# Optimization experiments

Measured on AMD Instinct MI355X. Metric: run time of the kernel, lower is better.

The kernel has to match this reference:

```python
import jax, jax.numpy as jnp
import numpy as np

B, T, D, H = 4, 2048, 1024, 16
E = D // H  # 64
DH = D // 4  # sensor hidden dim


def setup_inputs() -> dict:
    key = jax.random.key(0)
    ks = jax.random.split(key, 9)
    s = D ** -0.5
    return {
        "x": jax.random.normal(ks[0], (B, T, D), jnp.float32),
        "q_w": jax.random.normal(ks[1], (D, D), jnp.float32) * s,
        "k_w": jax.random.normal(ks[2], (D, D), jnp.float32) * s,
        "v_w": jax.random.normal(ks[3], (D, D), jnp.float32) * s,
        "o_w": jax.random.normal(ks[4], (D, D), jnp.float32) * s,
        "cs_w1": jax.random.normal(ks[5], (DH, D), jnp.float32) * s,
        "cs_b1": jnp.zeros((DH,), jnp.float32),
        "cs_w2": jax.random.normal(ks[6], (H, DH), jnp.float32) * (DH ** -0.5),
        "cs_b2": jnp.zeros((H,), jnp.float32),
        "decay_params": jax.random.normal(ks[7], (H, E), jnp.float32) + 3.0,
    }


def reference(x, q_w, k_w, v_w, o_w, cs_w1, cs_b1, cs_w2, cs_b2, decay_params):
    Bx, Tx, Dx = x.shape
    # projections (torch Linear: y = x @ W.T), split into heads
    q = (x @ q_w.T).reshape(Bx, Tx, H, E)
    k = (x @ k_w.T).reshape(Bx, Tx, H, E)
    v = (x @ v_w.T).reshape(Bx, Tx, H, E)
    # complexity sensor -> per-head scalar in (0,1)
    lc = jax.nn.sigmoid(jnp.tanh(x @ cs_w1.T + cs_b1) @ cs_w2.T + cs_b2)  # [B,T,H]
    base = jax.nn.sigmoid(decay_params)[None, None]                       # [1,1,H,E]
    lam = jnp.clip(base * (1.0 + 0.2 * lc[..., None]), 0.0, 0.9995)       # [B,T,H,E]

    def step(state, inp):
        qt, kt, vt, dt = inp  # each [B,H,E]
        # S(t) = diag(dt) S(t-1) + k_t v_t^T  (decay along key dim e)
        state = state * dt[..., None] + kt[..., None] * vt[:, :, None, :]
        out_t = jnp.einsum('bhe,bhef->bhf', qt, state)
        return state, out_t

    init = jnp.zeros((Bx, H, E, E), x.dtype)
    xs = (jnp.swapaxes(q, 0, 1), jnp.swapaxes(k, 0, 1),
          jnp.swapaxes(v, 0, 1), jnp.swapaxes(lam, 0, 1))  # time-major
    _, ys = jax.lax.scan(step, init, xs)  # ys: [T,B,H,E]
    y = jnp.swapaxes(ys, 0, 1).reshape(Bx, Tx, Dx)
    return y @ o_w.T
```

## Files before the change

### kernel.cpp

```cpp
#include <hip/hip_runtime.h>

#define DEV __device__ __forceinline__
#define MFMA(a, b, c) __builtin_amdgcn_mfma_f32_16x16x32_bf16(a, b, c, 0, 0, 0)

typedef __bf16 bf16x8 __attribute__((ext_vector_type(8)));
typedef float f32x4 __attribute__((ext_vector_type(4)));
typedef unsigned short u16x8 __attribute__((ext_vector_type(8)));

DEV float blo(unsigned u) { return __builtin_bit_cast(float, u << 16); }
DEV float bhi(unsigned u) { return __builtin_bit_cast(float, u & 0xFFFF0000u); }
DEV unsigned short f2b(float f) {
  unsigned u = __builtin_bit_cast(unsigned, f);
  return (unsigned short)((u + 0x7FFFu + ((u >> 16) & 1u)) >> 16);
}
DEV unsigned cvtpk(float lo, float hi) {
  unsigned r;
  asm("v_cvt_pk_bf16_f32 %0, %1, %2" : "=v"(r) : "v"(lo), "v"(hi));
  return r;
}
DEV float sigf(float x) { return 1.0f / (1.0f + expf(-x)); }

DEV void llds16(const void* g, void* l) {
  __builtin_amdgcn_global_load_lds(
      (__attribute__((address_space(1))) void*)(void*)g,
      (__attribute__((address_space(3))) void*)l, 16, 0, 0);
}

__global__ __launch_bounds__(256) void cvt_w_kernel(
    const float* __restrict__ qw, const float* __restrict__ kw,
    const float* __restrict__ vw, const float* __restrict__ cw1,
    const float* __restrict__ ow, unsigned short* __restrict__ WCAT,
    unsigned short* __restrict__ OWB) {
  const int i = blockIdx.x * 256 + threadIdx.x;
  const float* s;
  unsigned short* d;
  if (i < 262144)      { s = qw  + (size_t)i * 4;                 d = WCAT + (size_t)i * 4; }
  else if (i < 524288) { size_t j = i - 262144; s = kw  + j * 4;  d = WCAT + 1048576 + j * 4; }
  else if (i < 786432) { size_t j = i - 524288; s = vw  + j * 4;  d = WCAT + 2097152 + j * 4; }
  else if (i < 851968) { size_t j = i - 786432; s = cw1 + j * 4;  d = WCAT + 3145728 + j * 4; }
  else if (i < 1114112){ size_t j = i - 851968; s = ow  + j * 4;  d = OWB + j * 4; }
  else return;
  float4 f = *(const float4*)s;
  ushort4 o;
  o.x = f2b(f.x); o.y = f2b(f.y); o.z = f2b(f.z); o.w = f2b(f.w);
  *(ushort4*)d = o;
}

template <int OUTF, int AF32>
__global__ __launch_bounds__(256, 2) void gemm_bk64_kernel(
    const void* __restrict__ Ap, const unsigned short* __restrict__ B,
    void* __restrict__ Cout, unsigned short* __restrict__ Cout2,
    int K, int ldC, int act_col0, const float* __restrict__ bias, int nbn) {
  __shared__ char As[16384];
  __shared__ char Bs[16384];
  const int tid = threadIdx.x;
  const int lane = tid & 63;
  const int w = tid >> 6;
  const int wr = w >> 1, wc = w & 1;
  const int ln15 = lane & 15, hi = lane >> 4;

  const int nwg = gridDim.x, orig = blockIdx.x;
  const int qd = nwg >> 3, rm = nwg & 7;
  const int xcd = orig & 7, loc = orig >> 3;
  const int swz = (xcd < rm ? xcd * (qd + 1) : rm * (qd + 1) + (xcd - rm) * qd) + loc;
  const int bn = swz % nbn, bm = swz / nbn;
  const int m0 = bm * 128, n0 = bn * 128;

  auto stage = [&](const unsigned short* src, int row0, int k0, char* dst) {
#pragma unroll
    for (int j = 0; j < 4; ++j) {
      const int slot = j * 256 + tid;
      const int rr = slot >> 3;
      const int kc = (slot & 7) ^ (rr & 7);
      llds16(src + (size_t)(row0 + rr) * K + k0 + kc * 8, dst + slot * 16);
    }
  };
  auto stageA32 = [&](const float* src, int row0, int k0, char* dst) {
    float4 f[4][2];
#pragma unroll
    for (int j = 0; j < 4; ++j) {
      const int slot = j * 256 + tid;
      const int rr = slot >> 3;
      const int kc = (slot & 7) ^ (rr & 7);
      const float* g = src + (size_t)(row0 + rr) * K + k0 + kc * 8;
      f[j][0] = *(const float4*)g;
      f[j][1] = *(const float4*)(g + 4);
    }
#pragma unroll
    for (int j = 0; j < 4; ++j) {
      const int slot = j * 256 + tid;
      uint4 o = { cvtpk(f[j][0].x, f[j][0].y), cvtpk(f[j][0].z, f[j][0].w),
                  cvtpk(f[j][1].x, f[j][1].y), cvtpk(f[j][1].z, f[j][1].w) };
      *(uint4*)(dst + slot * 16) = o;
    }
  };
  auto rd = [&](const char* unit, int row, int ks) -> bf16x8 {
    const int kc = (ks * 4 + hi) ^ (row & 7);
    return *(const bf16x8*)(unit + row * 128 + kc * 16);
  };

  f32x4 acc[4][4] = {};
  const int nk = K >> 6;
  for (int kt = 0; kt < nk; ++kt) {
    if (AF32) stageA32((const float*)Ap, m0, kt * 64, As);
    else      stage((const unsigned short*)Ap, m0, kt * 64, As);
    stage(B, n0, kt * 64, Bs);
    __syncthreads();
    bf16x8 af[2][4], bf[2][4];
#pragma unroll
    for (int ks = 0; ks < 2; ++ks)
#pragma unroll
      for (int i = 0; i < 4; ++i) {
        af[ks][i] = rd(As, wr * 64 + i * 16 + ln15, ks);
        bf[ks][i] = rd(Bs, wc * 64 + i * 16 + ln15, ks);
      }
#pragma unroll
    for (int i = 0; i < 4; ++i)
#pragma unroll
      for (int j = 0; j < 4; ++j) {
        acc[i][j] = MFMA(af[0][i], bf[0][j], acc[i][j]);
        acc[i][j] = MFMA(af[1][i], bf[1][j], acc[i][j]);
      }
    __syncthreads();
  }
#pragma unroll
  for (int i = 0; i < 4; ++i) {
    const int rowb = m0 + wr * 64 + i * 16 + hi * 4;
#pragma unroll
    for (int j = 0; j < 4; ++j) {
      const int col = n0 + wc * 64 + j * 16 + ln15;
#pragma unroll
      for (int r = 0; r < 4; ++r) {
        float v = acc[i][j][r];
        if (col >= act_col0) {
          v = tanhf(v + bias[col - act_col0]);
          Cout2[(size_t)(rowb + r) * 256 + (col - act_col0)] = f2b(v);
        } else {
          const size_t off = (size_t)(rowb + r) * ldC + col;
          if (OUTF == 0) ((unsigned short*)Cout)[off] = f2b(v);
          else ((float*)Cout)[off] = v;
        }
      }
    }
  }
}

__global__ __launch_bounds__(256) void sensor2_kernel(
    const unsigned short* __restrict__ H1, const float* __restrict__ w2,
    const float* __restrict__ b2, float* __restrict__ LC) {
  const int tid = threadIdx.x;
  const int h = tid & 15, r = tid >> 4;
  const int m = blockIdx.x * 16 + r;
  const unsigned short* hrow = H1 + (size_t)m * 256;
  const float* wrow = w2 + h * 256;
  float acc = 0.0f;
  for (int d = 0; d < 256; d += 8) {
    uint4 hv = *(const uint4*)(hrow + d);
    float4 wa = *(const float4*)(wrow + d);
    float4 wb = *(const float4*)(wrow + d + 4);
    acc = fmaf(blo(hv.x), wa.x, acc); acc = fmaf(bhi(hv.x), wa.y, acc);
    acc = fmaf(blo(hv.y), wa.z, acc); acc = fmaf(bhi(hv.y), wa.w, acc);
    acc = fmaf(blo(hv.z), wb.x, acc); acc = fmaf(bhi(hv.z), wb.y, acc);
    acc = fmaf(blo(hv.w), wb.z, acc); acc = fmaf(bhi(hv.w), wb.w, acc);
  }
  LC[(size_t)m * 16 + h] = sigf(acc + b2[h]);
}

__global__ __launch_bounds__(256) void scan_passA_kernel(
    const unsigned short* __restrict__ QKV, const float* __restrict__ LC,
    const float* __restrict__ decay, unsigned short* __restrict__ MTB,
    float* __restrict__ P) {
  __shared__ char SH[34304];
  ushort* kL = (ushort*)SH;
  ushort* vL = (ushort*)(SH + 8192);
  char* khT  = SH + 16384;
  char* vT   = SH + 24576;
  float* sigL = (float*)(SH + 32768);
  float* lcL  = (float*)(SH + 33024);
  float* Lp   = (float*)(SH + 33280);

  const int tid = threadIdx.x;
  const int c = blockIdx.x, h = blockIdx.y, b = blockIdx.z;
  const int t0 = c * 64;
#pragma unroll
  for (int i = 0; i < 2; ++i) {
    int idx = i * 256 + tid;
    int row = idx >> 3, ch = idx & 7;
    size_t g = (size_t)(b * 2048 + t0 + row) * 3072 + h * 64 + ch * 8;
    int lb = (i * 256 + (tid >> 6) * 64) * 16;
    llds16(QKV + g + 1024, (char*)kL + lb);
    llds16(QKV + g + 2048, (char*)vL + lb);
  }
  if (tid < 64) sigL[tid] = sigf(decay[h * 64 + tid]);
  else if (tid < 128) lcL[tid - 64] = LC[(size_t)(b * 2048 + t0 + tid - 64) * 16 + h];
  __syncthreads();

  const int e = tid & 63, seg = tid >> 6;
  const float sig_e = sigL[e];
  float lp = 1.f;
#pragma unroll
  for (int i = 0; i < 16; ++i)
    lp *= fminf(sig_e * (1.f + 0.2f * lcL[seg * 16 + i]), 0.9995f);
  Lp[seg * 64 + e] = lp;
  __syncthreads();
  float T = 1.f;
#pragma unroll
  for (int sg = 0; sg < 4; ++sg) if (sg > seg) T *= Lp[sg * 64 + e];

  u16x8 ka = {}, kb = {};
  float r = T;
#pragma unroll
  for (int i = 15; i >= 0; --i) {
    int s = seg * 16 + i;
    float lam = fminf(sig_e * (1.f + 0.2f * lcL[s]), 0.9995f);
    float kv = blo((unsigned)kL[s * 64 + e]) * r;
    if (i >= 8) kb[i - 8] = f2b(kv); else ka[i] = f2b(kv);
    r *= lam;
  }
  *(u16x8*)(khT + e * 128 + (((2 * seg + 0) ^ (e & 7)) * 16)) = ka;
  *(u16x8*)(khT + e * 128 + (((2 * seg + 1) ^ (e & 7)) * 16)) = kb;
  if (seg == 0) P[((size_t)((b * 16 + h) * 32 + c)) * 64 + e] = r;

  u16x8 va = {}, vb = {};
#pragma unroll
  for (int i = 0; i < 16; ++i) {
    unsigned short vv = vL[(seg * 16 + i) * 64 + e];
    if (i >= 8) vb[i - 8] = vv; else va[i] = vv;
  }
  *(u16x8*)(vT + e * 128 + (((2 * seg + 0) ^ (e & 7)) * 16)) = va;
  *(u16x8*)(vT + e * 128 + (((2 * seg + 1) ^ (e & 7)) * 16)) = vb;
  __syncthreads();

  const int ln15 = tid & 15, hi = (tid & 63) >> 4, w = tid >> 6;
  auto rd = [&](const char* u, int row, int ks) -> bf16x8 {
    return *(const bf16x8*)(u + row * 128 + (((ks * 4 + hi) ^ (row & 7)) * 16));
  };
  bf16x8 av0 = rd(vT, w * 16 + ln15, 0), av1 = rd(vT, w * 16 + ln15, 1);
  unsigned short* Mp = MTB + ((size_t)((b * 16 + h) * 32 + c)) * 4096;
#pragma unroll
  for (int er = 0; er < 4; ++er) {
    f32x4 acc = {};
    acc = MFMA(av0, rd(khT, er * 16 + ln15, 0), acc);
    acc = MFMA(av1, rd(khT, er * 16 + ln15, 1), acc);
    const int e2 = er * 16 + ln15;
#pragma unroll
    for (int rr = 0; rr < 4; ++rr) {
      const int f = w * 16 + hi * 4 + rr;
      Mp[f * 64 + (((e2 >> 3) ^ (f & 7)) << 3) + (e2 & 7)] = f2b(acc[rr]);
    }
  }
}

__global__ __launch_bounds__(256) void scan_passB_kernel(
    unsigned short* __restrict__ MTB, const float* __restrict__ P) {
  const int bh = blockIdx.y;
  const int task = blockIdx.x * 256 + threadIdx.x;
  const int f = task >> 6, slot = (task >> 3) & 7, pos = task & 7;
  const int e = ((slot ^ (f & 7)) << 3) | pos;
  const size_t base = (size_t)bh * 32;
  float S = 0.0f;
  for (int c = 0; c < 32; ++c) {
    unsigned short* Mp = MTB + (base + c) * 4096 + task;
    const float p = P[(base + c) * 64 + e];
    const float m = blo((unsigned)*Mp);
    *Mp = f2b(S);
    S = fmaf(p, S, m);
  }
}

__global__ __launch_bounds__(256) void scan_passC_kernel(
    const unsigned short* __restrict__ QKV, const float* __restrict__ LC,
    const float* __restrict__ decay, const unsigned short* __restrict__ MTB,
    unsigned short* __restrict__ Y) {
  __shared__ char SH[50688];
  ushort* qL = (ushort*)SH;
  ushort* kL = (ushort*)(SH + 8192);
  ushort* vL = (ushort*)(SH + 16384);
  char* qT = SH + 24576;
  char* kT = SH + 32768;
  char* vT = SH + 40960;
  char* Ab   = SH;
  char* sinT = SH + 8192;
  float* sigL = (float*)(SH + 49152);
  float* lcL  = (float*)(SH + 49408);
  float* Lp   = (float*)(SH + 49664);

  const int tid = threadIdx.x;
  const int c = blockIdx.x, h = blockIdx.y, b = blockIdx.z;
  const int t0 = c * 64;
#pragma unroll
  for (int i = 0; i < 2; ++i) {
    int idx = i * 256 + tid;
    int row = idx >> 3, ch = idx & 7;
    size_t g = (size_t)(b * 2048 + t0 + row) * 3072 + h * 64 + ch * 8;
    int lb = (i * 256 + (tid >> 6) * 64) * 16;
    llds16(QKV + g,        (char*)qL + lb);
    llds16(QKV + g + 1024, (char*)kL + lb);
    llds16(QKV + g + 2048, (char*)vL + lb);
  }
  if (tid < 64) sigL[tid] = sigf(decay[h * 64 + tid]);
  else if (tid < 128) lcL[tid - 64] = LC[(size_t)(b * 2048 + t0 + tid - 64) * 16 + h];
  __syncthreads();

  const int e = tid & 63, seg = tid >> 6;
  const float sig_e = sigL[e];
  float lp = 1.f;
#pragma unroll
  for (int i = 0; i < 16; ++i)
    lp *= fminf(sig_e * (1.f + 0.2f * lcL[seg * 16 + i]), 0.9995f);
  Lp[seg * 64 + e] = lp;
  __syncthreads();
  float a = 1.f;
#pragma unroll
  for (int sg = 0; sg < 4; ++sg) if (sg < seg) a *= Lp[sg * 64 + e];

#pragma unroll
  for (int i = 0; i < 16; ++i) {
    int t = seg * 16 + i;
    a *= fminf(sig_e * (1.f + 0.2f * lcL[t]), 0.9995f);
    float qv = blo((unsigned)qL[t * 64 + e]) * a;
    float kv = blo((unsigned)kL[t * 64 + e]) / fmaxf(a, 1e-30f);
    int off = ((e >> 3) ^ (t & 7)) * 16 + (e & 7) * 2;
    *(unsigned short*)(qT + t * 128 + off) = f2b(qv);
    *(unsigned short*)(kT + t * 128 + off) = f2b(kv);
  }
  u16x8 va = {}, vb = {};
#pragma unroll
  for (int i = 0; i < 16; ++i) {
    unsigned short vv = vL[(seg * 16 + i) * 64 + e];
    if (i >= 8) vb[i - 8] = vv; else va[i] = vv;
  }
  *(u16x8*)(vT + e * 128 + (((2 * seg + 0) ^ (e & 7)) * 16)) = va;
  *(u16x8*)(vT + e * 128 + (((2 * seg + 1) ^ (e & 7)) * 16)) = vb;
  __syncthreads();

  {
    const unsigned short* Ms = MTB + ((size_t)((b * 16 + h) * 32 + c)) * 4096;
#pragma unroll
    for (int i = 0; i < 2; ++i)
      llds16(Ms + (size_t)(i * 256 + tid) * 8, sinT + (i * 256 + (tid >> 6) * 64) * 16);
  }
  const int ln15 = tid & 15, hi = (tid & 63) >> 4, w = tid >> 6;
  auto rd = [&](const char* u, int row, int ks) -> bf16x8 {
    return *(const bf16x8*)(u + row * 128 + (((ks * 4 + hi) ^ (row & 7)) * 16));
  };
  bf16x8 Aq0 = rd(qT, w * 16 + ln15, 0), Aq1 = rd(qT, w * 16 + ln15, 1);
  f32x4 acc1[4];
#pragma unroll
  for (int sr = 0; sr < 4; ++sr) {
    acc1[sr] = (f32x4){0.f, 0.f, 0.f, 0.f};
    if (sr <= w) {
      acc1[sr] = MFMA(Aq0, rd(kT, sr * 16 + ln15, 0), acc1[sr]);
      acc1[sr] = MFMA(Aq1, rd(kT, sr * 16 + ln15, 1), acc1[sr]);
    }
  }
#pragma unroll
  for (int sr = 0; sr < 4; ++sr)
#pragma unroll
    for (int rr = 0; rr < 4; ++rr) {
      int t = w * 16 + hi * 4 + rr;
      int s = sr * 16 + ln15;
      float v = 0.f;
      if (sr <= w && s <= t) v = acc1[sr][rr];
      *(unsigned short*)(Ab + t * 128 + (((s >> 3) ^ (t & 7)) * 16) + (s & 7) * 2) = f2b(v);
    }
  bf16x8 Aa0 = rd(Ab, w * 16 + ln15, 0), Aa1 = rd(Ab, w * 16 + ln15, 1);
  __syncthreads();

  f32x4 accY[4];
#pragma unroll
  for (int fr = 0; fr < 4; ++fr) {
    accY[fr] = (f32x4){0.f, 0.f, 0.f, 0.f};
    accY[fr] = MFMA(Aq0, rd(sinT, fr * 16 + ln15, 0), accY[fr]);
    accY[fr] = MFMA(Aq1, rd(sinT, fr * 16 + ln15, 1), accY[fr]);
    accY[fr] = MFMA(Aa0, rd(vT, fr * 16 + ln15, 0), accY[fr]);
    accY[fr] = MFMA(Aa1, rd(vT, fr * 16 + ln15, 1), accY[fr]);
  }
#pragma unroll
  for (int fr = 0; fr < 4; ++fr)
#pragma unroll
    for (int rr = 0; rr < 4; ++rr)
      Y[(size_t)(b * 2048 + t0 + w * 16 + hi * 4 + rr) * 1024 + h * 64 + fr * 16 + ln15]
        = f2b(accY[fr][rr]);
}

extern "C" void kernel_launch(void* const* d_in, const int* in_sizes, int n_in,
                              void* d_out, int out_size, void* d_ws, size_t ws_size,
                              hipStream_t stream) {
  (void)in_sizes; (void)n_in; (void)out_size; (void)ws_size;
  const float* x     = (const float*)d_in[0];
  const float* q_w   = (const float*)d_in[1];
  const float* k_w   = (const float*)d_in[2];
  const float* v_w   = (const float*)d_in[3];
  const float* o_w   = (const float*)d_in[4];
  const float* cs_w1 = (const float*)d_in[5];
  const float* cs_b1 = (const float*)d_in[6];
  const float* cs_w2 = (const float*)d_in[7];
  const float* cs_b2 = (const float*)d_in[8];
  const float* decay = (const float*)d_in[9];
  float* out = (float*)d_out;

  char* ws = (char*)d_ws;
  unsigned short* WCAT = (unsigned short*)(ws + 16777216);
  unsigned short* OWB  = (unsigned short*)(ws + 23592960);
  unsigned short* QKV  = (unsigned short*)(ws + 25690112);
  unsigned short* H1   = (unsigned short*)(ws + 76021760);
  float*          LCb  = (float*)(ws + 80216064);
  unsigned short* MTB  = (unsigned short*)(ws + 80740352);
  float*          Pb   = (float*)(ws + 97517568);
  unsigned short* YB   = (unsigned short*)(ws + 98041856);

  cvt_w_kernel<<<4352, 256, 0, stream>>>(q_w, k_w, v_w, cs_w1, o_w, WCAT, OWB);

  gemm_bk64_kernel<0, 1><<<1664, 256, 0, stream>>>(x, WCAT, QKV, H1,
                                                   1024, 3072, 3072, cs_b1, 26);
  sensor2_kernel<<<512, 256, 0, stream>>>(H1, cs_w2, cs_b2, LCb);

  scan_passA_kernel<<<dim3(32, 16, 4), 256, 0, stream>>>(QKV, LCb, decay, MTB, Pb);
  scan_passB_kernel<<<dim3(16, 64), 256, 0, stream>>>(MTB, Pb);
  scan_passC_kernel<<<dim3(32, 16, 4), 256, 0, stream>>>(QKV, LCb, decay, MTB, YB);

  gemm_bk64_kernel<1, 0><<<512, 256, 0, stream>>>(YB, OWB, out, nullptr,
                                                  1024, 1024, 1 << 30, nullptr, 8);
}
```

Measured before the change: 181.4 us.

## Stage fp32 A tiles via direct-to-LDS loads and cut per-step divisions in chunk prep

For the fp32-input GEMM variant, A tiles are now copied straight into a doubled LDS buffer with global_load_lds, and converted to bf16 when fragments are read, instead of going through registers and converting before the LDS store. This removes register staging and VGPR pressure on the global load path, but doubles A's LDS footprint and moves the conversion into the inner loop. In the chunk scan prep, decay factors are computed once, and the key scaling uses a reverse cumulative product times one reciprocal in place of a division per element, which slightly changes the numerics.

```diff
diff --git a/kernel.cpp b/kernel.cpp
--- a/kernel.cpp
+++ b/kernel.cpp
@@ -51,7 +51,7 @@
     const void* __restrict__ Ap, const unsigned short* __restrict__ B,
     void* __restrict__ Cout, unsigned short* __restrict__ Cout2,
     int K, int ldC, int act_col0, const float* __restrict__ bias, int nbn) {
-  __shared__ char As[16384];
+  __shared__ char As[AF32 ? 32768 : 16384];
   __shared__ char Bs[16384];
   const int tid = threadIdx.x;
   const int lane = tid & 63;
@@ -75,34 +75,33 @@
       llds16(src + (size_t)(row0 + rr) * K + k0 + kc * 8, dst + slot * 16);
     }
   };
-  auto stageA32 = [&](const float* src, int row0, int k0, char* dst) {
-    float4 f[4][2];
-#pragma unroll
-    for (int j = 0; j < 4; ++j) {
+  auto stageA32 = [&](const float* src, int row0, int k0) {
+#pragma unroll
+    for (int j = 0; j < 8; ++j) {
       const int slot = j * 256 + tid;
-      const int rr = slot >> 3;
-      const int kc = (slot & 7) ^ (rr & 7);
-      const float* g = src + (size_t)(row0 + rr) * K + k0 + kc * 8;
-      f[j][0] = *(const float4*)g;
-      f[j][1] = *(const float4*)(g + 4);
-    }
-#pragma unroll
-    for (int j = 0; j < 4; ++j) {
-      const int slot = j * 256 + tid;
-      uint4 o = { cvtpk(f[j][0].x, f[j][0].y), cvtpk(f[j][0].z, f[j][0].w),
-                  cvtpk(f[j][1].x, f[j][1].y), cvtpk(f[j][1].z, f[j][1].w) };
-      *(uint4*)(dst + slot * 16) = o;
+      const int rr = slot >> 4;
+      const int sc = (slot & 15) ^ (rr & 15);
+      llds16(src + (size_t)(row0 + rr) * K + k0 + sc * 4, As + slot * 16);
     }
   };
   auto rd = [&](const char* unit, int row, int ks) -> bf16x8 {
     const int kc = (ks * 4 + hi) ^ (row & 7);
     return *(const bf16x8*)(unit + row * 128 + kc * 16);
   };
+  auto rdA32 = [&](int row, int ks) -> bf16x8 {
+    const int s1 = (2 * (ks * 4 + hi)) ^ (row & 15);
+    const f32x4 p0 = *(const f32x4*)(As + row * 256 + s1 * 16);
+    const f32x4 p1 = *(const f32x4*)(As + row * 256 + (s1 ^ 1) * 16);
+    union { unsigned u[4]; bf16x8 v; } o;
+    o.u[0] = cvtpk(p0[0], p0[1]); o.u[1] = cvtpk(p0[2], p0[3]);
+    o.u[2] = cvtpk(p1[0], p1[1]); o.u[3] = cvtpk(p1[2], p1[3]);
+    return o.v;
+  };
 
   f32x4 acc[4][4] = {};
   const int nk = K >> 6;
   for (int kt = 0; kt < nk; ++kt) {
-    if (AF32) stageA32((const float*)Ap, m0, kt * 64, As);
+    if (AF32) stageA32((const float*)Ap, m0, kt * 64);
     else      stage((const unsigned short*)Ap, m0, kt * 64, As);
     stage(B, n0, kt * 64, Bs);
     __syncthreads();
@@ -111,7 +110,8 @@
     for (int ks = 0; ks < 2; ++ks)
 #pragma unroll
       for (int i = 0; i < 4; ++i) {
-        af[ks][i] = rd(As, wr * 64 + i * 16 + ln15, ks);
+        af[ks][i] = AF32 ? rdA32(wr * 64 + i * 16 + ln15, ks)
+                         : rd(As, wr * 64 + i * 16 + ln15, ks);
         bf[ks][i] = rd(Bs, wc * 64 + i * 16 + ln15, ks);
       }
 #pragma unroll
@@ -304,24 +304,36 @@
 
   const int e = tid & 63, seg = tid >> 6;
   const float sig_e = sigL[e];
+  float lam[16];
+#pragma unroll
+  for (int i = 0; i < 16; ++i)
+    lam[i] = fminf(sig_e * (1.f + 0.2f * lcL[seg * 16 + i]), 0.9995f);
   float lp = 1.f;
 #pragma unroll
-  for (int i = 0; i < 16; ++i)
-    lp *= fminf(sig_e * (1.f + 0.2f * lcL[seg * 16 + i]), 0.9995f);
+  for (int i = 0; i < 16; ++i) lp *= lam[i];
   Lp[seg * 64 + e] = lp;
   __syncthreads();
   float a = 1.f;
 #pragma unroll
   for (int sg = 0; sg < 4; ++sg) if (sg < seg) a *= Lp[sg * 64 + e];
 
+  float ap = a;
 #pragma unroll
   for (int i = 0; i < 16; ++i) {
     int t = seg * 16 + i;
-    a *= fminf(sig_e * (1.f + 0.2f * lcL[t]), 0.9995f);
-    float qv = blo((unsigned)qL[t * 64 + e]) * a;
-    float kv = blo((unsigned)kL[t * 64 + e]) / fmaxf(a, 1e-30f);
+    ap *= lam[i];
+    float qv = blo((unsigned)qL[t * 64 + e]) * ap;
     int off = ((e >> 3) ^ (t & 7)) * 16 + (e & 7) * 2;
     *(unsigned short*)(qT + t * 128 + off) = f2b(qv);
+  }
+  const float inv_end = 1.0f / ap;
+  float R = 1.f;
+#pragma unroll
+  for (int i = 15; i >= 0; --i) {
+    int t = seg * 16 + i;
+    float kv = blo((unsigned)kL[t * 64 + e]) * (R * inv_end);
+    R *= lam[i];
+    int off = ((e >> 3) ^ (t & 7)) * 16 + (e & 7) * 2;
     *(unsigned short*)(kT + t * 128 + off) = f2b(kv);
   }
   u16x8 va = {}, vb = {};
```

Result: slower. 185.2 us (+2.1%).
